# Performance work log

Hardware: AMD Instinct MI355X
Metric: run time of the kernel (lower is better)

Reference implementation:

```python
import jax, jax.numpy as jnp
import numpy as np
import math

D = 512      # d_model
HEADS = 16   # num_heads
HD = 32      # head_dim
WS = 7       # window_size
KS = 8       # patch_size
S = 4        # spectral_stride


def dct_basis(n):
    k = np.arange(n, dtype=np.float64)[:, None]
    i = np.arange(n, dtype=np.float64)[None, :]
    B = np.cos(np.pi * (i + 0.5) * k / n)
    B[0, :] *= 1.0 / np.sqrt(2.0)
    B = B * np.sqrt(2.0 / n)
    return jnp.asarray(B, dtype=jnp.float32)


def setup_inputs() -> dict:
    key = jax.random.key(0)
    ks = jax.random.split(key, 24)
    Bb, H, W = 4, 112, 112
    N = H * W
    w = lambda k, shape: jax.random.normal(k, shape, jnp.float32) * 0.02
    return {
        'tokens': jax.random.normal(ks[0], (Bb, N, D), jnp.float32),
        'patches': jax.random.normal(ks[1], (Bb, 3 * KS * KS, N), jnp.float32),
        'Wq': w(ks[2], (D, D)), 'bq': w(ks[3], (D,)),
        'Wk': w(ks[4], (D, D)), 'bk': w(ks[5], (D,)),
        'Wv': w(ks[6], (D, D)), 'bv': w(ks[7], (D,)),
        'Wo': w(ks[8], (D, D)), 'bo': w(ks[9], (D,)),
        'Wsp': w(ks[10], (3 * KS * KS, D)), 'bsp': w(ks[11], (D,)),
        'Wsq': w(ks[12], (D, D)), 'bsq': w(ks[13], (D,)),
        'Wsk': w(ks[14], (D, D)), 'bsk': w(ks[15], (D,)),
        'Wsv': w(ks[16], (D, D)), 'bsv': w(ks[17], (D,)),
        'Wso': w(ks[18], (D, D)), 'bso': w(ks[19], (D,)),
        'alpha': jnp.asarray(0.5, jnp.float32),
        'H': H, 'W': W,
    }


def reference(tokens, patches, Wq, bq, Wk, bk, Wv, bv, Wo, bo,
              Wsp, bsp, Wsq, bsq, Wsk, bsk, Wsv, bsv, Wso, bso,
              alpha, H, W):
    B, N, d = tokens.shape
    # ---- local windowed multi-head attention ----
    ws = WS
    pad_h = (-H) % ws
    pad_w = (-W) % ws
    x = tokens.reshape(B, H, W, d)
    if pad_h or pad_w:
        x = jnp.pad(x, ((0, 0), (0, pad_h), (0, pad_w), (0, 0)))
    Hp, Wp = H + pad_h, W + pad_w
    nh, nw_ = Hp // ws, Wp // ws
    xw = x.reshape(B, nh, ws, nw_, ws, d).transpose(0, 1, 3, 2, 4, 5)
    xw = xw.reshape(B * nh * nw_, ws * ws, d)  # (nw, 49, d)
    nw, L, _ = xw.shape
    q = (xw @ Wq + bq).reshape(nw, L, HEADS, HD)
    k = (xw @ Wk + bk).reshape(nw, L, HEADS, HD)
    v = (xw @ Wv + bv).reshape(nw, L, HEADS, HD)
    scale = 1.0 / math.sqrt(HD)
    attn = jax.nn.softmax(jnp.einsum('nqhd,nkhd->nhqk', q, k) * scale, axis=-1)
    o = jnp.einsum('nhqk,nkhd->nqhd', attn, v).reshape(nw, L, d)
    o = o @ Wo + bo
    o = o.reshape(B, nh, nw_, ws, ws, d).transpose(0, 1, 3, 2, 4, 5).reshape(B, Hp, Wp, d)
    sp_out = o[:, :H, :W, :].reshape(B, N, d)
    # ---- DCT on raw patches -> spectral descriptors ----
    Bm = dct_basis(KS)
    p = patches.reshape(B, 3, KS, KS, N)
    Fc = jnp.einsum('ij,bcjkn->bcikn', Bm, p)
    Fc = jnp.einsum('bcijn,jk->bcikn', Fc, Bm)  # right-multiply by Bm^T transposed back
    spec_desc = Fc.reshape(B, 3 * KS * KS, N).transpose(0, 2, 1) @ Wsp + bsp  # (B,N,d)
    # ---- strided global spectral attention + nearest upsample ----
    spec_hw = spec_desc.reshape(B, H, W, d)
    sd = spec_hw[:, ::S, ::S, :]
    Hs, Ws = sd.shape[1], sd.shape[2]
    sd = sd.reshape(B, Hs * Ws, d)
    qs = sd @ Wsq + bsq
    ks_ = sd @ Wsk + bsk
    vs = sd @ Wsv + bsv
    a = jax.nn.softmax(jnp.einsum('bqd,bkd->bqk', qs, ks_) / math.sqrt(d), axis=-1)
    so = jnp.einsum('bqk,bkd->bqd', a, vs) @ Wso + bso
    so = so.reshape(B, Hs, Ws, d)
    ri = (jnp.arange(H) * Hs) // H  # torch nearest: floor(i*in/out)
    ci = (jnp.arange(W) * Ws) // W
    spec_out = so[:, ri][:, :, ci].reshape(B, N, d)
    # ---- fuse + residual + layernorm (no affine) ----
    al = jax.nn.sigmoid(alpha)
    out = tokens + al * sp_out + (1.0 - al) * spec_out
    mu = out.mean(-1, keepdims=True)
    var = ((out - mu) ** 2).mean(-1, keepdims=True)
    return (out - mu) / jnp.sqrt(var + 1e-5)
```

## Files before the change

kernel.cpp:

```cpp
#include <hip/hip_runtime.h>

typedef unsigned short u16;
typedef __attribute__((ext_vector_type(4))) float f32x4;
typedef __attribute__((ext_vector_type(8))) short bf16x8;

#define AS1 __attribute__((address_space(1)))
#define AS3 __attribute__((address_space(3)))
#define GLL(gp, lp) __builtin_amdgcn_global_load_lds((const AS1 void*)(gp), (AS3 void*)(lp), 16, 0, 0)

__device__ __forceinline__ float b2f(u16 v) { return __uint_as_float(((unsigned)v) << 16); }
__device__ __forceinline__ u16 f2b(float f) {
  unsigned u = __float_as_uint(f);
  u += 0x7fffu + ((u >> 16) & 1u);
  return (u16)(u >> 16);
}
__device__ __forceinline__ unsigned pack2(float a, float b) {
  return (unsigned)f2b(a) | ((unsigned)f2b(b) << 16);
}
__device__ __forceinline__ float blo(unsigned u) { return __uint_as_float(u << 16); }
__device__ __forceinline__ float bhi(unsigned u) { return __uint_as_float(u & 0xffff0000u); }

__global__ __launch_bounds__(256) void gemm_bt(
    const u16* __restrict__ A, int lda, long sAb,
    const u16* __restrict__ Bt, int ldb, long sBb,
    const float* __restrict__ bias, void* __restrict__ Cv, int ldc, long sCb,
    int M, int N, int K, int c_bf16)
{
  __shared__ __align__(16) u16 ldsA[128 * 64];
  __shared__ __align__(16) u16 ldsB[128 * 64];
  int tid = threadIdx.x;
  int wid = tid >> 6, lane = tid & 63;
  int row0 = blockIdx.y << 7;
  int col0 = blockIdx.x << 7;
  int bz = blockIdx.z;
  A += (size_t)bz * sAb;
  Bt += (size_t)bz * sBb;
  int wr = (wid >> 1) << 6, wc = (wid & 1) << 6;

  f32x4 acc[4][4];
#pragma unroll
  for (int i = 0; i < 4; ++i)
#pragma unroll
    for (int j = 0; j < 4; ++j) { f32x4 z = {0.f, 0.f, 0.f, 0.f}; acc[i][j] = z; }

  for (int kt = 0; kt < K; kt += 64) {
#pragma unroll
    for (int q = 0; q < 4; ++q) {
      int inst = (wid << 2) + q;
      int o = (inst << 10) + (lane << 4);
      int r = o >> 7;
      int cs = (o >> 4) & 7;
      int cl = cs ^ (r & 7);
      int ar = row0 + r; ar = ar < M ? ar : M - 1;
      GLL(A + (size_t)ar * lda + kt + (cl << 3), ldsA + (inst << 9));
      int br = col0 + r; br = br < N ? br : N - 1;
      GLL(Bt + (size_t)br * ldb + kt + (cl << 3), ldsB + (inst << 9));
    }
    __syncthreads();
#pragma unroll
    for (int kk = 0; kk < 2; ++kk) {
      bf16x8 af[4], bg[4];
#pragma unroll
      for (int mi = 0; mi < 4; ++mi) {
        int r = wr + (mi << 4) + (lane & 15);
        int cs = ((kk << 2) + (lane >> 4)) ^ (r & 7);
        af[mi] = *(const bf16x8*)(ldsA + (r << 6) + (cs << 3));
      }
#pragma unroll
      for (int ni = 0; ni < 4; ++ni) {
        int r = wc + (ni << 4) + (lane & 15);
        int cs = ((kk << 2) + (lane >> 4)) ^ (r & 7);
        bg[ni] = *(const bf16x8*)(ldsB + (r << 6) + (cs << 3));
      }
#pragma unroll
      for (int mi = 0; mi < 4; ++mi)
#pragma unroll
        for (int ni = 0; ni < 4; ++ni)
          acc[mi][ni] = __builtin_amdgcn_mfma_f32_16x16x32_bf16(af[mi], bg[ni], acc[mi][ni], 0, 0, 0);
    }
    __syncthreads();
  }

#pragma unroll
  for (int mi = 0; mi < 4; ++mi) {
    int rb = row0 + wr + (mi << 4) + ((lane >> 4) << 2);
#pragma unroll
    for (int ni = 0; ni < 4; ++ni) {
      int c = col0 + wc + (ni << 4) + (lane & 15);
      float bv = (bias && c < N) ? bias[c] : 0.f;
#pragma unroll
      for (int j = 0; j < 4; ++j) {
        int r = rb + j;
        if (r < M && c < N) {
          float v = acc[mi][ni][j] + bv;
          if (c_bf16) ((u16*)Cv)[(size_t)bz * sCb + (size_t)r * ldc + c] = f2b(v);
          else ((float*)Cv)[(size_t)bz * sCb + (size_t)r * ldc + c] = v;
        }
      }
    }
  }
}

__global__ __launch_bounds__(256, 2) void win_attn_mfma(const u16* __restrict__ qkv, u16* __restrict__ oat)
{
  __shared__ __align__(16) u16 Pl[4][64 * 72];
  __shared__ __align__(16) u16 Vtl[4][32 * 72];
  int tid = threadIdx.x;
  int wid = tid >> 6, lane = tid & 63;
  int lm = lane & 15, lg = lane >> 4;
  int w = blockIdx.x;
  int b = w >> 8, wh = (w >> 4) & 15, ww = w & 15;
  int rowbase = (wh * 7) * 112 + ww * 7;
  u16* P = Pl[wid];
  u16* Vt = Vtl[wid];
  const u16* base = qkv + (size_t)b * 12544 * 1536;
  u16* ob = oat + (size_t)b * 12544 * 512;
  const float scale = 0.17677669529663687f;

  for (int hh = 0; hh < 4; ++hh) {
    int h = wid * 4 + hh;
    bf16x8 Qf[4], Kf[4];
#pragma unroll
    for (int mi = 0; mi < 4; ++mi) {
      int i = mi * 16 + lm; i = i < 49 ? i : 48;
      int q7 = (i * 147) >> 10;
      int n = rowbase + q7 * 112 + (i - q7 * 7);
      const u16* rp = base + (size_t)n * 1536 + h * 32 + lg * 8;
      Qf[mi] = *(const bf16x8*)(rp);
      Kf[mi] = *(const bf16x8*)(rp + 512);
    }
    {
      int j = lane;
      if (j < 49) {
        int q7 = (j * 147) >> 10;
        int n = rowbase + q7 * 112 + (j - q7 * 7);
        const uint4* vp = (const uint4*)(base + (size_t)n * 1536 + 1024 + h * 32);
#pragma unroll
        for (int t = 0; t < 4; ++t) {
          uint4 u = vp[t];
          Vt[(t * 8 + 0) * 72 + j] = (u16)(u.x & 0xffff); Vt[(t * 8 + 1) * 72 + j] = (u16)(u.x >> 16);
          Vt[(t * 8 + 2) * 72 + j] = (u16)(u.y & 0xffff); Vt[(t * 8 + 3) * 72 + j] = (u16)(u.y >> 16);
          Vt[(t * 8 + 4) * 72 + j] = (u16)(u.z & 0xffff); Vt[(t * 8 + 5) * 72 + j] = (u16)(u.z >> 16);
          Vt[(t * 8 + 6) * 72 + j] = (u16)(u.w & 0xffff); Vt[(t * 8 + 7) * 72 + j] = (u16)(u.w >> 16);
        }
      } else {
#pragma unroll
        for (int d = 0; d < 32; ++d) Vt[d * 72 + j] = 0;
      }
    }
    f32x4 S[4][4];
#pragma unroll
    for (int mi = 0; mi < 4; ++mi)
#pragma unroll
      for (int nj = 0; nj < 4; ++nj) { f32x4 z = {0.f, 0.f, 0.f, 0.f}; S[mi][nj] = z; }
#pragma unroll
    for (int mi = 0; mi < 4; ++mi)
#pragma unroll
      for (int nj = 0; nj < 4; ++nj)
        S[mi][nj] = __builtin_amdgcn_mfma_f32_16x16x32_bf16(Qf[mi], Kf[nj], S[mi][nj], 0, 0, 0);
    float invv[4][4];
#pragma unroll
    for (int mi = 0; mi < 4; ++mi) {
#pragma unroll
      for (int reg = 0; reg < 4; ++reg) {
        float v0 = S[mi][0][reg], v1 = S[mi][1][reg], v2 = S[mi][2][reg], v3 = S[mi][3][reg];
        if (lm) v3 = -1e30f;
        float m = fmaxf(fmaxf(v0, v1), fmaxf(v2, v3));
#pragma unroll
        for (int o = 1; o < 16; o <<= 1) m = fmaxf(m, __shfl_xor(m, o));
        float e0 = __expf((v0 - m) * scale);
        float e1 = __expf((v1 - m) * scale);
        float e2 = __expf((v2 - m) * scale);
        float e3 = lm ? 0.f : __expf((v3 - m) * scale);
        float s = e0 + e1 + e2 + e3;
#pragma unroll
        for (int o = 1; o < 16; o <<= 1) s += __shfl_xor(s, o);
        invv[mi][reg] = 1.f / s;
        int r = mi * 16 + lg * 4 + reg;
        P[r * 72 + lm] = f2b(e0);
        P[r * 72 + 16 + lm] = f2b(e1);
        P[r * 72 + 32 + lm] = f2b(e2);
        P[r * 72 + 48 + lm] = f2b(e3);
      }
    }
    bf16x8 Vf[2][2];
#pragma unroll
    for (int dt = 0; dt < 2; ++dt) {
      Vf[dt][0] = *(const bf16x8*)(Vt + (dt * 16 + lm) * 72 + lg * 8);
      Vf[dt][1] = *(const bf16x8*)(Vt + (dt * 16 + lm) * 72 + 32 + lg * 8);
    }
    f32x4 O[4][2];
#pragma unroll
    for (int mi = 0; mi < 4; ++mi)
#pragma unroll
      for (int dt = 0; dt < 2; ++dt) { f32x4 z = {0.f, 0.f, 0.f, 0.f}; O[mi][dt] = z; }
#pragma unroll
    for (int mi = 0; mi < 4; ++mi) {
      bf16x8 Pf0 = *(const bf16x8*)(P + (mi * 16 + lm) * 72 + lg * 8);
      bf16x8 Pf1 = *(const bf16x8*)(P + (mi * 16 + lm) * 72 + 32 + lg * 8);
#pragma unroll
      for (int dt = 0; dt < 2; ++dt) {
        O[mi][dt] = __builtin_amdgcn_mfma_f32_16x16x32_bf16(Pf0, Vf[dt][0], O[mi][dt], 0, 0, 0);
        O[mi][dt] = __builtin_amdgcn_mfma_f32_16x16x32_bf16(Pf1, Vf[dt][1], O[mi][dt], 0, 0, 0);
      }
    }
#pragma unroll
    for (int mi = 0; mi < 4; ++mi)
#pragma unroll
      for (int reg = 0; reg < 4; ++reg) {
        int i = mi * 16 + lg * 4 + reg;
        if (i < 49) {
          int q7 = (i * 147) >> 10;
          int n = rowbase + q7 * 112 + (i - q7 * 7);
          float iv = invv[mi][reg];
          u16* op = ob + (size_t)n * 512 + h * 32 + lm;
          op[0] = f2b(O[mi][0][reg] * iv);
          op[16] = f2b(O[mi][1][reg] * iv);
        }
      }
  }
}

__global__ __launch_bounds__(192) void dct_f2(const float* __restrict__ patches, u16* __restrict__ F2)
{
  __shared__ float pv[192];
  __shared__ float Bm[64];
  int blk = blockIdx.x;
  int b = blk / 784, rem = blk % 784;
  int n = ((rem / 28) * 4) * 112 + (rem % 28) * 4;
  int t = threadIdx.x;
  if (t < 64) {
    int k = t >> 3, ii = t & 7;
    float v = cosf(3.14159265358979323846f * (ii + 0.5f) * (float)k * 0.125f) * 0.5f;
    if (k == 0) v *= 0.70710678118654752f;
    Bm[t] = v;
  }
  pv[t] = patches[((size_t)b * 192 + t) * 12544 + n];
  __syncthreads();
  int c = t >> 6, fi = (t >> 3) & 7, fk = t & 7;
  float acc = 0.f;
#pragma unroll
  for (int mm = 0; mm < 8; ++mm) {
    float g = 0.f;
#pragma unroll
    for (int jj = 0; jj < 8; ++jj) g += pv[c * 64 + mm * 8 + jj] * Bm[jj * 8 + fk];
    acc += Bm[fi * 8 + mm] * g;
  }
  F2[(size_t)blk * 192 + t] = f2b(acc);
}

__global__ __launch_bounds__(256) void spec_softmax(const float* __restrict__ S, u16* __restrict__ P)
{
  __shared__ float red[4];
  int row = blockIdx.x;
  const float* sr = S + (size_t)row * 784;
  u16* pr = P + (size_t)row * 832;
  int t = threadIdx.x;
  int lane = t & 63, wid = t >> 6;
  float v0 = sr[t];
  float v1 = sr[t + 256];
  float v2 = (t < 272) ? sr[t + 512] : -1e30f;
  float m = fmaxf(fmaxf(v0, v1), v2);
#pragma unroll
  for (int ofs = 32; ofs > 0; ofs >>= 1) m = fmaxf(m, __shfl_xor(m, ofs));
  if (lane == 0) red[wid] = m;
  __syncthreads();
  m = fmaxf(fmaxf(red[0], red[1]), fmaxf(red[2], red[3]));
  __syncthreads();
  const float scale = 0.044194173824159216f;
  float e0 = __expf((v0 - m) * scale);
  float e1 = __expf((v1 - m) * scale);
  float e2 = (t < 272) ? __expf((v2 - m) * scale) : 0.f;
  float sum = e0 + e1 + e2;
#pragma unroll
  for (int ofs = 32; ofs > 0; ofs >>= 1) sum += __shfl_xor(sum, ofs);
  if (lane == 0) red[wid] = sum;
  __syncthreads();
  sum = red[0] + red[1] + red[2] + red[3];
  float inv = 1.f / sum;
  pr[t] = f2b(e0 * inv);
  pr[t + 256] = f2b(e1 * inv);
  if (t < 272) pr[t + 512] = f2b(e2 * inv);
  else if (t < 320) pr[t + 512] = 0;
}

__global__ __launch_bounds__(256) void transV(const u16* __restrict__ qkvs, u16* __restrict__ Vt)
{
  int idx = blockIdx.x * 256 + threadIdx.x;
  int k = idx % 832;
  int rest = idx / 832;
  int n = rest % 512, b = rest / 512;
  u16 v = 0;
  if (k < 784) v = qkvs[((size_t)(b * 784 + k)) * 1536 + 1024 + n];
  Vt[idx] = v;
}

__global__ __launch_bounds__(256) void combine_ln(
    const float* __restrict__ tokens, const u16* __restrict__ sp,
    const float* __restrict__ so, const float* __restrict__ alpha,
    float* __restrict__ out)
{
  int nidx = blockIdx.x;
  int b = nidx / 12544, pos = nidx % 12544;
  int i = pos / 112, j = pos % 112;
  const float* tr = tokens + (size_t)nidx * 512;
  const u16* sr = sp + (size_t)nidx * 512;
  const float* qr = so + (size_t)(b * 784 + (i >> 2) * 28 + (j >> 2)) * 512;
  float al = 1.f / (1.f + __expf(-alpha[0]));
  float be = 1.f - al;
  int t = threadIdx.x;
  float x0 = tr[t] + al * b2f(sr[t]) + be * qr[t];
  float x1 = tr[t + 256] + al * b2f(sr[t + 256]) + be * qr[t + 256];
  float s = x0 + x1, ss = x0 * x0 + x1 * x1;
#pragma unroll
  for (int ofs = 32; ofs > 0; ofs >>= 1) { s += __shfl_xor(s, ofs); ss += __shfl_xor(ss, ofs); }
  __shared__ float rs[4], rq[4];
  int lane = t & 63, wid = t >> 6;
  if (lane == 0) { rs[wid] = s; rq[wid] = ss; }
  __syncthreads();
  s = rs[0] + rs[1] + rs[2] + rs[3];
  ss = rq[0] + rq[1] + rq[2] + rq[3];
  float mu = s * 0.001953125f;
  float var = ss * 0.001953125f - mu * mu;
  float rstd = rsqrtf(var + 1e-5f);
  float* orow = out + (size_t)nidx * 512;
  orow[t] = (x0 - mu) * rstd;
  orow[t + 256] = (x1 - mu) * rstd;
}

__global__ __launch_bounds__(256) void transT(const float* __restrict__ src, u16* __restrict__ dst, int K, int Nc)
{
  int idx = blockIdx.x * 256 + threadIdx.x;
  if (idx >= K * Nc) return;
  int nn = idx / K, kk = idx % K;
  dst[idx] = f2b(src[(size_t)kk * Nc + nn]);
}

__global__ __launch_bounds__(256) void cvtbf(const float* __restrict__ src, u16* __restrict__ dst)
{
  size_t i = ((size_t)blockIdx.x * 256 + threadIdx.x) * 4;
  float4 v = *(const float4*)(src + i);
  uint2 u;
  u.x = pack2(v.x, v.y);
  u.y = pack2(v.z, v.w);
  *(uint2*)(dst + i) = u;
}

__global__ __launch_bounds__(256) void stack_bias(
    const float* bq_, const float* bk_, const float* bv_,
    const float* bsq_, const float* bsk_, const float* bsv_,
    float* bqkv, float* bsqkv)
{
  int i = blockIdx.x * 256 + threadIdx.x;
  if (i >= 1536) return;
  int r = i & 511;
  bqkv[i]  = (i < 512) ? bq_[r]  : (i < 1024) ? bk_[r]  : bv_[r];
  bsqkv[i] = (i < 512) ? bsq_[r] : (i < 1024) ? bsk_[r] : bsv_[r];
}

extern "C" void kernel_launch(void* const* d_in, const int* in_sizes, int n_in,
                              void* d_out, int out_size, void* d_ws, size_t ws_size,
                              hipStream_t stream) {
  (void)in_sizes; (void)n_in; (void)out_size; (void)ws_size;
  const float* tokens = (const float*)d_in[0];
  const float* patches = (const float*)d_in[1];
  const float* Wq  = (const float*)d_in[2];
  const float* bq  = (const float*)d_in[3];
  const float* Wk  = (const float*)d_in[4];
  const float* bk  = (const float*)d_in[5];
  const float* Wv  = (const float*)d_in[6];
  const float* bv  = (const float*)d_in[7];
  const float* Wo  = (const float*)d_in[8];
  const float* bo  = (const float*)d_in[9];
  const float* Wsp = (const float*)d_in[10];
  const float* bsp = (const float*)d_in[11];
  const float* Wsq = (const float*)d_in[12];
  const float* bsq = (const float*)d_in[13];
  const float* Wsk = (const float*)d_in[14];
  const float* bsk = (const float*)d_in[15];
  const float* Wsv = (const float*)d_in[16];
  const float* bsv = (const float*)d_in[17];
  const float* Wso = (const float*)d_in[18];
  const float* bso = (const float*)d_in[19];
  const float* alpha = (const float*)d_in[20];
  float* out = (float*)d_out;

  char* ws = (char*)d_ws;
  u16* tokbf  = (u16*)ws;
  u16* qkv    = (u16*)(ws + 51380224);
  char* pp    = ws + 51380224 + 154140672;
  u16* WqkvT  = (u16*)pp; pp += 1572864;
  u16* WoT    = (u16*)pp; pp += 524288;
  u16* WsqkvT = (u16*)pp; pp += 1572864;
  u16* WsoT   = (u16*)pp; pp += 524288;
  u16* WspT   = (u16*)pp; pp += 196608;
  float* bqkv = (float*)pp; pp += 6144;
  float* bsqkv= (float*)pp; pp += 6144;
  u16* F2b    = (u16*)pp; pp += 1204224;
  u16* sd     = (u16*)pp; pp += 3211264;
  u16* qkvs   = (u16*)pp; pp += 9633792;
  u16* sopre  = (u16*)pp; pp += 3211264;
  float* sofin= (float*)pp; pp += 6422528;

  float* Sbuf = (float*)tokbf;
  u16* Pbuf   = (u16*)(ws + 9834496);
  u16* Vt     = (u16*)(ws + 9834496 + 5218304);

  cvtbf<<<25088, 256, 0, stream>>>(tokens, tokbf);
  transT<<<1024, 256, 0, stream>>>(Wq, WqkvT, 512, 512);
  transT<<<1024, 256, 0, stream>>>(Wk, WqkvT + 262144, 512, 512);
  transT<<<1024, 256, 0, stream>>>(Wv, WqkvT + 524288, 512, 512);
  transT<<<1024, 256, 0, stream>>>(Wo, WoT, 512, 512);
  transT<<<1024, 256, 0, stream>>>(Wsq, WsqkvT, 512, 512);
  transT<<<1024, 256, 0, stream>>>(Wsk, WsqkvT + 262144, 512, 512);
  transT<<<1024, 256, 0, stream>>>(Wsv, WsqkvT + 524288, 512, 512);
  transT<<<1024, 256, 0, stream>>>(Wso, WsoT, 512, 512);
  transT<<<384, 256, 0, stream>>>(Wsp, WspT, 192, 512);
  stack_bias<<<6, 256, 0, stream>>>(bq, bk, bv, bsq, bsk, bsv, bqkv, bsqkv);

  gemm_bt<<<dim3(12, 392), 256, 0, stream>>>(tokbf, 512, 0, WqkvT, 512, 0, bqkv, qkv, 1536, 0, 50176, 1536, 512, 1);
  win_attn_mfma<<<1024, 256, 0, stream>>>(qkv, tokbf);
  gemm_bt<<<dim3(4, 392), 256, 0, stream>>>(tokbf, 512, 0, WoT, 512, 0, bo, qkv, 512, 0, 50176, 512, 512, 1);

  dct_f2<<<3136, 192, 0, stream>>>(patches, F2b);
  gemm_bt<<<dim3(4, 25), 256, 0, stream>>>(F2b, 192, 0, WspT, 192, 0, bsp, sd, 512, 0, 3136, 512, 192, 1);
  gemm_bt<<<dim3(12, 25), 256, 0, stream>>>(sd, 512, 0, WsqkvT, 512, 0, bsqkv, qkvs, 1536, 0, 3136, 1536, 512, 1);
  gemm_bt<<<dim3(7, 7, 4), 256, 0, stream>>>(qkvs, 1536, (long)784 * 1536, qkvs + 512, 1536, (long)784 * 1536,
                                             nullptr, Sbuf, 784, (long)784 * 784, 784, 784, 512, 0);
  spec_softmax<<<3136, 256, 0, stream>>>(Sbuf, Pbuf);
  transV<<<6656, 256, 0, stream>>>(qkvs, Vt);
  gemm_bt<<<dim3(4, 7, 4), 256, 0, stream>>>(Pbuf, 832, (long)784 * 832, Vt, 832, (long)512 * 832,
                                             nullptr, sopre, 512, (long)784 * 512, 784, 512, 832, 1);
  gemm_bt<<<dim3(4, 25), 256, 0, stream>>>(sopre, 512, 0, WsoT, 512, 0, bso, sofin, 512, 0, 3136, 512, 512, 0);

  combine_ln<<<50176, 256, 0, stream>>>(tokens, qkv, sofin, alpha, out);
}
```

Before: 540.8 us.

## Double-buffer GEMM LDS tiles and remap workgroups across XCDs

The bf16 MFMA GEMM now keeps two LDS buffers and issues the global-to-LDS loads for the next K tile before computing on the current one, so memory latency can overlap with MFMA work. Global source pointers and LDS offsets are computed once before the K loop instead of on every iteration. Block indices are remapped so that consecutive tiles land on the same XCD, which should improve L2 reuse. LDS use doubles to 64 KB per block, which may lower occupancy.

```diff
diff --git a/kernel.cpp b/kernel.cpp
--- a/kernel.cpp
+++ b/kernel.cpp
@@ -26,37 +26,69 @@
     const float* __restrict__ bias, void* __restrict__ Cv, int ldc, long sCb,
     int M, int N, int K, int c_bf16)
 {
-  __shared__ __align__(16) u16 ldsA[128 * 64];
-  __shared__ __align__(16) u16 ldsB[128 * 64];
+  __shared__ __align__(16) u16 ldsA[2][128 * 64];
+  __shared__ __align__(16) u16 ldsB[2][128 * 64];
   int tid = threadIdx.x;
   int wid = tid >> 6, lane = tid & 63;
-  int row0 = blockIdx.y << 7;
-  int col0 = blockIdx.x << 7;
+
+  int nbx = gridDim.x;
+  int lin = blockIdx.y * nbx + blockIdx.x;
+  int nwg = nbx * gridDim.y;
+  int qc = nwg >> 3, rc = nwg & 7;
+  int xcd = lin & 7, pos = lin >> 3;
+  int nlin = (xcd < rc ? xcd * (qc + 1) : rc * (qc + 1) + (xcd - rc) * qc) + pos;
+  int bx = nlin % nbx, by = nlin / nbx;
+
+  int row0 = by << 7;
+  int col0 = bx << 7;
   int bz = blockIdx.z;
   A += (size_t)bz * sAb;
   Bt += (size_t)bz * sBb;
   int wr = (wid >> 1) << 6, wc = (wid & 1) << 6;
 
+  const u16* pA[4];
+  const u16* pB[4];
+  int ldso[4];
+#pragma unroll
+  for (int q = 0; q < 4; ++q) {
+    int inst = (wid << 2) + q;
+    int o = (inst << 10) + (lane << 4);
+    int r = o >> 7;
+    int cs = (o >> 4) & 7;
+    int cl = cs ^ (r & 7);
+    int ar = row0 + r; ar = ar < M ? ar : M - 1;
+    int br = col0 + r; br = br < N ? br : N - 1;
+    pA[q] = A + (size_t)ar * lda + (cl << 3);
+    pB[q] = Bt + (size_t)br * ldb + (cl << 3);
+    ldso[q] = inst << 9;
+  }
+
   f32x4 acc[4][4];
 #pragma unroll
   for (int i = 0; i < 4; ++i)
 #pragma unroll
     for (int j = 0; j < 4; ++j) { f32x4 z = {0.f, 0.f, 0.f, 0.f}; acc[i][j] = z; }
 
-  for (int kt = 0; kt < K; kt += 64) {
-#pragma unroll
-    for (int q = 0; q < 4; ++q) {
-      int inst = (wid << 2) + q;
-      int o = (inst << 10) + (lane << 4);
-      int r = o >> 7;
-      int cs = (o >> 4) & 7;
-      int cl = cs ^ (r & 7);
-      int ar = row0 + r; ar = ar < M ? ar : M - 1;
-      GLL(A + (size_t)ar * lda + kt + (cl << 3), ldsA + (inst << 9));
-      int br = col0 + r; br = br < N ? br : N - 1;
-      GLL(Bt + (size_t)br * ldb + kt + (cl << 3), ldsB + (inst << 9));
-    }
-    __syncthreads();
+#pragma unroll
+  for (int q = 0; q < 4; ++q) {
+    GLL(pA[q], &ldsA[0][ldso[q]]);
+    GLL(pB[q], &ldsB[0][ldso[q]]);
+    pA[q] += 64; pB[q] += 64;
+  }
+  __syncthreads();
+
+  int nt = K >> 6;
+  int cur = 0;
+  for (int t = 0; t < nt; ++t) {
+    if (t + 1 < nt) {
+      int nxt = cur ^ 1;
+#pragma unroll
+      for (int q = 0; q < 4; ++q) {
+        GLL(pA[q], &ldsA[nxt][ldso[q]]);
+        GLL(pB[q], &ldsB[nxt][ldso[q]]);
+        pA[q] += 64; pB[q] += 64;
+      }
+    }
 #pragma unroll
     for (int kk = 0; kk < 2; ++kk) {
       bf16x8 af[4], bg[4];
@@ -64,13 +96,13 @@
       for (int mi = 0; mi < 4; ++mi) {
         int r = wr + (mi << 4) + (lane & 15);
         int cs = ((kk << 2) + (lane >> 4)) ^ (r & 7);
-        af[mi] = *(const bf16x8*)(ldsA + (r << 6) + (cs << 3));
+        af[mi] = *(const bf16x8*)(&ldsA[cur][(r << 6) + (cs << 3)]);
       }
 #pragma unroll
       for (int ni = 0; ni < 4; ++ni) {
         int r = wc + (ni << 4) + (lane & 15);
         int cs = ((kk << 2) + (lane >> 4)) ^ (r & 7);
-        bg[ni] = *(const bf16x8*)(ldsB + (r << 6) + (cs << 3));
+        bg[ni] = *(const bf16x8*)(&ldsB[cur][(r << 6) + (cs << 3)]);
       }
 #pragma unroll
       for (int mi = 0; mi < 4; ++mi)
@@ -79,6 +111,7 @@
           acc[mi][ni] = __builtin_amdgcn_mfma_f32_16x16x32_bf16(af[mi], bg[ni], acc[mi][ni], 0, 0, 0);
     }
     __syncthreads();
+    cur ^= 1;
   }
 
 #pragma unroll
```

After: 578.5 us. 1.07x slower.
